# Optimization experiments

Measured on AMD Instinct MI355X. Metric: run time of the kernel, lower is better.

The kernel has to match this reference:

```python
import jax, jax.numpy as jnp
import numpy as np

N_GRAPHS = 200
NODES_PER_GRAPH = 500
N_NODES = N_GRAPHS * NODES_PER_GRAPH  # 100000
N_EDGES = 1_600_000
INPUT_DIM = 64
GCN_DIM = 128
SEQ_LEN = 20
LSTM_DIM = 128
OUTPUT_DIM = 1


def setup_inputs() -> dict:
    key = jax.random.key(0)
    ks = jax.random.split(key, 10)
    # edges constrained to stay inside each graph (block-diagonal adjacency)
    src = jax.random.randint(ks[0], (N_EDGES,), 0, N_NODES, dtype=jnp.int32)
    dst_local = jax.random.randint(ks[1], (N_EDGES,), 0, NODES_PER_GRAPH, dtype=jnp.int32)
    dst = (src // NODES_PER_GRAPH) * NODES_PER_GRAPH + dst_local
    graph_ids = jnp.arange(N_NODES, dtype=jnp.int32) // NODES_PER_GRAPH
    x = jax.random.normal(ks[2], (N_NODES, INPUT_DIM), dtype=jnp.float32)
    s = 0.05
    w_gcn = jax.random.normal(ks[3], (INPUT_DIM, GCN_DIM), dtype=jnp.float32) * s
    b_gcn = jnp.zeros((GCN_DIM,), dtype=jnp.float32)
    w_ih = jax.random.normal(ks[4], (4 * LSTM_DIM, GCN_DIM), dtype=jnp.float32) * s
    w_hh = jax.random.normal(ks[5], (4 * LSTM_DIM, LSTM_DIM), dtype=jnp.float32) * s
    b_ih = jax.random.normal(ks[6], (4 * LSTM_DIM,), dtype=jnp.float32) * s
    b_hh = jax.random.normal(ks[7], (4 * LSTM_DIM,), dtype=jnp.float32) * s
    w_fc = jax.random.normal(ks[8], (OUTPUT_DIM, LSTM_DIM), dtype=jnp.float32) * s
    b_fc = jnp.zeros((OUTPUT_DIM,), dtype=jnp.float32)
    return {"x": x, "src": src, "dst": dst, "graph_ids": graph_ids,
            "w_gcn": w_gcn, "b_gcn": b_gcn, "w_ih": w_ih, "w_hh": w_hh,
            "b_ih": b_ih, "b_hh": b_hh, "w_fc": w_fc, "b_fc": b_fc}


def reference(x, src, dst, graph_ids, w_gcn, b_gcn, w_ih, w_hh, b_ih, b_hh, w_fc, b_fc):
    ones_e = jnp.ones((src.shape[0],), dtype=x.dtype)
    # DGL GraphConv norm='both': D_out^{-1/2} on src side, D_in^{-1/2} on dst side,
    # degrees clamped to min 1 (allow_zero_in_degree=True)
    out_deg = jnp.clip(jax.ops.segment_sum(ones_e, src, num_segments=N_NODES), 1.0)
    in_deg = jnp.clip(jax.ops.segment_sum(ones_e, dst, num_segments=N_NODES), 1.0)
    h = x * (out_deg ** -0.5)[:, None]                               # [N, Din]
    agg = jax.ops.segment_sum(h[src], dst, num_segments=N_NODES)     # gather+scatter-add
    h = agg * (in_deg ** -0.5)[:, None]
    h = jnp.maximum(h @ w_gcn + b_gcn, 0.0)                           # [N, GCN_DIM], ReLU
    # dgl.mean_nodes: per-graph mean pool
    cnt = jax.ops.segment_sum(jnp.ones((N_NODES,), h.dtype), graph_ids, num_segments=N_GRAPHS)
    hg = jax.ops.segment_sum(h, graph_ids, num_segments=N_GRAPHS) / cnt[:, None]  # [T, D]
    # build_dataset: sliding windows of length SEQ_LEN over the graph time series
    B = N_GRAPHS - SEQ_LEN + 1
    idx = jnp.arange(B)[:, None] + jnp.arange(SEQ_LEN)[None, :]
    dat = hg[idx]                                                      # [B, L, D]
    # single-layer LSTM (PyTorch gate order i,f,g,o), zero initial state
    x_proj = jnp.einsum('bld,gd->blg', dat, w_ih) + b_ih               # [B, L, 4H]
    h0 = jnp.zeros((B, LSTM_DIM), dat.dtype)
    c0 = jnp.zeros((B, LSTM_DIM), dat.dtype)

    def step(carry, xt):
        hprev, cprev = carry
        gates = xt + hprev @ w_hh.T + b_hh
        i, f, g, o = jnp.split(gates, 4, axis=-1)
        c = jax.nn.sigmoid(f) * cprev + jax.nn.sigmoid(i) * jnp.tanh(g)
        hh = jax.nn.sigmoid(o) * jnp.tanh(c)
        return (hh, c), None

    (h_n, _), _ = jax.lax.scan(step, (h0, c0), jnp.swapaxes(x_proj, 0, 1))
    pred = h_n @ w_fc.T + b_fc                                         # [B, OUTPUT_DIM]
    return pred
```

## Files before the change

### kernel.cpp

```cpp
#include <hip/hip_runtime.h>
#include <hip/hip_bf16.h>

#define N_GRAPHS 200
#define NPG      500
#define NPGP     512
#define N_NODES_ 100000
#define N_EDGES_ 1600000
#define DIN      64
#define DG       128
#define SEQ      20
#define HL       128
#define G4       512
#define BWIN     (N_GRAPHS - SEQ + 1)
#define NPART    512
#define EPB      (N_EDGES_/NPART)
#define SLOTS    48
#define CAP      9216

typedef __attribute__((ext_vector_type(8))) short short8;
typedef __attribute__((ext_vector_type(4))) float float4v;
typedef __attribute__((ext_vector_type(2))) _Float16 half2v;

__device__ __forceinline__ float sigmoidf_(float v){ return 1.0f/(1.0f+expf(-v)); }

__device__ __forceinline__ unsigned short f2bf(float f) {
  unsigned int u = __float_as_uint(f);
  u += 0x7fffu + ((u >> 16) & 1u);
  return (unsigned short)(u >> 16);
}

__device__ __forceinline__ float h2dot(half2v a, half2v b, float c) {
#if __has_builtin(__builtin_amdgcn_fdot2)
  return __builtin_amdgcn_fdot2(a, b, c, false);
#else
  return c + (float)a.x*(float)b.x + (float)a.y*(float)b.y;
#endif
}

__global__ __launch_bounds__(256) void k_part(const int* __restrict__ src,
                                              const int* __restrict__ dst,
                                              const float* __restrict__ w_hh,
                                              int* __restrict__ gcount,
                                              int* __restrict__ part,
                                              int4* __restrict__ whh16) {
  __shared__ int cnt[N_GRAPHS];
  __shared__ int base[N_GRAPHS];
  __shared__ int buf[N_GRAPHS][SLOTS];
  int b = blockIdx.x, t = threadIdx.x;
  if (b < 32) {
    int i = b*256 + t;
    int k4 = i >> 9, r = i & 511;
    const float4* wp = (const float4*)(w_hh + (size_t)r*HL + k4*8);
    float4 w0 = wp[0], w1 = wp[1];
    half2v p0 = {(_Float16)w0.x, (_Float16)w0.y};
    half2v p1 = {(_Float16)w0.z, (_Float16)w0.w};
    half2v p2 = {(_Float16)w1.x, (_Float16)w1.y};
    half2v p3 = {(_Float16)w1.z, (_Float16)w1.w};
    int4 pk;
    pk.x = __builtin_bit_cast(int, p0); pk.y = __builtin_bit_cast(int, p1);
    pk.z = __builtin_bit_cast(int, p2); pk.w = __builtin_bit_cast(int, p3);
    whh16[i] = pk;
  }
  for (int g = t; g < N_GRAPHS; g += 256) cnt[g] = 0;
  __syncthreads();
  int e0 = b*EPB;
  for (int i = t; i < EPB; i += 256) {
    int s = src[e0+i], d = dst[e0+i];
    int g = s / NPG;
    int pk = ((s - g*NPG) << 9) | (d - g*NPG);
    int pos = atomicAdd(&cnt[g], 1);
    if (pos < SLOTS) buf[g][pos] = pk;
    else { int gp = atomicAdd(&gcount[g], 1); part[g*CAP + gp] = pk; }
  }
  __syncthreads();
  if (t < N_GRAPHS) base[t] = atomicAdd(&gcount[t], min(cnt[t], SLOTS));
  __syncthreads();
  int w = t >> 6, lane = t & 63;
  for (int g = w; g < N_GRAPHS; g += 4) {
    int n = min(cnt[g], SLOTS);
    if (lane < n) part[g*CAP + base[g] + lane] = buf[g][lane];
  }
}

__global__ __launch_bounds__(512) void k_sort(const int* __restrict__ gcount,
    const int* __restrict__ part,
    unsigned short* __restrict__ sorted_all,
    int* __restrict__ e_end, int* __restrict__ e_deg,
    float* __restrict__ so_g) {
  __shared__ int indeg[512], outdeg[512], off[512];
  __shared__ int wsum[8];
  __shared__ int eC[CAP];
  __shared__ unsigned short sl[CAP];
  int g = blockIdx.x, t = threadIdx.x;
  int lane = t & 63, w = t >> 6;
  indeg[t] = 0; outdeg[t] = 0;
  __syncthreads();
  int nseg = gcount[g], seg0 = g*CAP;
  for (int e = t; e < nseg; e += 512) {
    int p = part[seg0 + e];
    eC[e] = p;
    atomicAdd(&indeg[p & 511], 1);
    atomicAdd(&outdeg[p >> 9], 1);
  }
  __syncthreads();
  int v = indeg[t], sc = v;
  #pragma unroll
  for (int o = 1; o < 64; o <<= 1) { int nn = __shfl_up(sc, o); if (lane >= o) sc += nn; }
  if (lane == 63) wsum[w] = sc;
  __syncthreads();
  int woff = 0;
  #pragma unroll
  for (int i = 0; i < 8; ++i) woff += (i < w) ? wsum[i] : 0;
  off[t] = woff + sc - v;
  so_g[g*512 + t] = rsqrtf((float)max(outdeg[t], 1));
  if (t < NPG) e_deg[g*NPG + t] = v;
  __syncthreads();
  for (int e = t; e < nseg; e += 512) {
    int p = eC[e];
    int pos = atomicAdd(&off[p & 511], 1);
    sl[pos] = (unsigned short)(p >> 9);
  }
  __syncthreads();
  if (t < NPG) e_end[g*NPG + t] = seg0 + off[t];
  int n4 = nseg >> 2;
  ushort4* dv = (ushort4*)(sorted_all + seg0);
  const ushort4* sv = (const ushort4*)sl;
  for (int i = t; i < n4; i += 512) dv[i] = sv[i];
  for (int i = (n4 << 2) + t; i < nseg; i += 512) sorted_all[seg0 + i] = sl[i];
}

__global__ __launch_bounds__(512, 1) void k_aggcn(
    const float* __restrict__ x, const float* __restrict__ so_g,
    const int* __restrict__ e_end, const int* __restrict__ e_deg,
    const unsigned short* __restrict__ sorted_all,
    const float* __restrict__ w_gcn, const float* __restrict__ b_gcn,
    const float* __restrict__ w_ih, const float* __restrict__ b_ih,
    float* __restrict__ proj) {
  __shared__ __align__(16) int4 xs[4008];
  __shared__ __align__(16) int4 hpre[4096];
  __shared__ unsigned short wLds[8192];
  __shared__ float pS[1024];
  __shared__ __align__(16) float hgS[128];
  int g = blockIdx.x, t = threadIdx.x;
  int lane = t & 63, w = t >> 6;
  const float4* xg = ((const float4*)x) + (size_t)g*8000;
  const float* sog = so_g + g*512;
  ushort4* xd = (ushort4*)xs;
  for (int i = t; i < 8000; i += 512) {
    float4 vv = xg[i];
    float s2 = sog[i >> 4];
    ushort4 u;
    u.x = f2bf(vv.x*s2); u.y = f2bf(vv.y*s2); u.z = f2bf(vv.z*s2); u.w = f2bf(vv.w*s2);
    xd[i] = u;
  }
  if (t < 16) xd[8000 + t] = make_ushort4(0,0,0,0);
  for (int i = t; i < 2048; i += 512) {
    float4 w4 = ((const float4*)w_gcn)[i];
    int k = i >> 5, c4 = (i & 31) << 2;
    int h = k >> 5, j = k & 7, lhi = ((k >> 3) & 3) << 4;
    float vvv[4] = {w4.x, w4.y, w4.z, w4.w};
    #pragma unroll
    for (int u = 0; u < 4; ++u) {
      int n = c4 + u;
      int idx = ((n >> 4)*2 + h)*64 + lhi + (n & 15);
      wLds[idx*8 + j] = f2bf(vvv[u]);
    }
  }
  __syncthreads();
  int g8 = lane >> 3, fl = lane & 7;
  int G = w*8 + g8;
  for (int sI = 0; sI < 8; ++sI) {
    int nl = sI*64 + G;
    int4 outv = make_int4(0,0,0,0);
    if (nl < NPG) {
      int n = g*NPG + nl;
      int end = e_end[n], dgr = e_deg[n], st = end - dgr;
      float aHi[4] = {0.f,0.f,0.f,0.f};
      float aLo[4] = {0.f,0.f,0.f,0.f};
      int ev = (fl < dgr) ? (int)sorted_all[st + fl] : 500;
      for (int c0 = 0; c0 < dgr; c0 += 8) {
        int nc = c0 + 8;
        int evn = (nc + fl < dgr) ? (int)sorted_all[st + nc + fl] : 500;
        #pragma unroll
        for (int j = 0; j < 8; ++j) {
          int se = __shfl(ev, (g8 << 3) + j);
          int4 vv = xs[(se << 3) + fl];
          aHi[0] += __uint_as_float((unsigned)vv.x & 0xffff0000u);
          aLo[0] += __uint_as_float((unsigned)vv.x << 16);
          aHi[1] += __uint_as_float((unsigned)vv.y & 0xffff0000u);
          aLo[1] += __uint_as_float((unsigned)vv.y << 16);
          aHi[2] += __uint_as_float((unsigned)vv.z & 0xffff0000u);
          aLo[2] += __uint_as_float((unsigned)vv.z << 16);
          aHi[3] += __uint_as_float((unsigned)vv.w & 0xffff0000u);
          aLo[3] += __uint_as_float((unsigned)vv.w << 16);
        }
        ev = evn;
      }
      float sn = rsqrtf((float)max(dgr, 1));
      outv.x = (int)(((unsigned)f2bf(aLo[0]*sn)) | ((unsigned)f2bf(aHi[0]*sn) << 16));
      outv.y = (int)(((unsigned)f2bf(aLo[1]*sn)) | ((unsigned)f2bf(aHi[1]*sn) << 16));
      outv.z = (int)(((unsigned)f2bf(aLo[2]*sn)) | ((unsigned)f2bf(aHi[2]*sn) << 16));
      outv.w = (int)(((unsigned)f2bf(aLo[3]*sn)) | ((unsigned)f2bf(aHi[3]*sn) << 16));
    }
    hpre[(nl << 3) + (fl ^ (nl & 7))] = outv;
  }
  __syncthreads();
  int quad = lane >> 4, l15 = lane & 15;
  float bcol[8];
  #pragma unroll
  for (int nt = 0; nt < 8; ++nt) bcol[nt] = b_gcn[nt*16 + l15];
  float psum[8] = {0.f,0.f,0.f,0.f,0.f,0.f,0.f,0.f};
  for (int i = 0; i < 4; ++i) {
    int row0 = (w + 8*i) << 4;
    int r = row0 + l15;
    int4 a0i = hpre[(r << 3) + (quad ^ (r & 7))];
    int4 a1i = hpre[(r << 3) + ((quad + 4) ^ (r & 7))];
    short8 a0 = *(const short8*)&a0i;
    short8 a1 = *(const short8*)&a1i;
    #pragma unroll
    for (int nt = 0; nt < 8; ++nt) {
      short8 b0 = *((const short8*)&wLds[((nt*2+0)*64 + lane)*8]);
      short8 b1 = *((const short8*)&wLds[((nt*2+1)*64 + lane)*8]);
      float4v acc = {0.f, 0.f, 0.f, 0.f};
      acc = __builtin_amdgcn_mfma_f32_16x16x32_bf16(a0, b0, acc, 0, 0, 0);
      acc = __builtin_amdgcn_mfma_f32_16x16x32_bf16(a1, b1, acc, 0, 0, 0);
      #pragma unroll
      for (int r4 = 0; r4 < 4; ++r4) {
        int node = row0 + quad*4 + r4;
        float vvv = acc[r4] + bcol[nt];
        psum[nt] += (node < NPG) ? fmaxf(vvv, 0.f) : 0.f;
      }
    }
  }
  #pragma unroll
  for (int nt = 0; nt < 8; ++nt) {
    float vvv = psum[nt];
    vvv += __shfl_xor(vvv, 16);
    vvv += __shfl_xor(vvv, 32);
    if (lane < 16) pS[w*DG + nt*16 + lane] = vvv;
  }
  __syncthreads();
  if (t < DG) {
    float sum = 0.f;
    #pragma unroll
    for (int w8 = 0; w8 < 8; ++w8) sum += pS[w8*DG + t];
    hgS[t] = sum * (1.0f/NPG);
  }
  __syncthreads();
  const float4* wr = (const float4*)(w_ih + (size_t)t*HL);
  const float4* hv = (const float4*)hgS;
  float acc = b_ih[t];
  #pragma unroll
  for (int k4 = 0; k4 < 32; ++k4) {
    float4 w4 = wr[k4]; float4 h4 = hv[k4];
    acc += w4.x*h4.x + w4.y*h4.y + w4.z*h4.z + w4.w*h4.w;
  }
  proj[(size_t)g*G4 + t] = acc;
}

__global__ __launch_bounds__(512) void k_lstm(const float* __restrict__ proj,
    const int4* __restrict__ whh16, const float* __restrict__ b_hh,
    const float* __restrict__ w_fc, const float* __restrict__ b_fc,
    float* __restrict__ out) {
  __shared__ float gS[G4];
  __shared__ __align__(16) int4 hPi[16];
  int b = blockIdx.x, t = threadIdx.x;
  int4 W[16];
  #pragma unroll
  for (int k4 = 0; k4 < 16; ++k4) W[k4] = whh16[(k4 << 9) + t];
  if (t < 16) hPi[t] = make_int4(0,0,0,0);
  float bh = b_hh[t];
  float c0 = 0.f, c1 = 0.f;
  __syncthreads();
  for (int l = 0; l < SEQ; ++l) {
    float a0 = proj[(size_t)(b+l)*G4 + t] + bh;
    float a1 = 0.f, a2 = 0.f, a3 = 0.f;
    #pragma unroll
    for (int k4 = 0; k4 < 16; k4 += 4) {
      int4 hv0 = hPi[k4+0]; int4 hv1 = hPi[k4+1];
      int4 hv2 = hPi[k4+2]; int4 hv3 = hPi[k4+3];
      a0 = h2dot(__builtin_bit_cast(half2v, W[k4+0].x), __builtin_bit_cast(half2v, hv0.x), a0);
      a0 = h2dot(__builtin_bit_cast(half2v, W[k4+0].y), __builtin_bit_cast(half2v, hv0.y), a0);
      a0 = h2dot(__builtin_bit_cast(half2v, W[k4+0].z), __builtin_bit_cast(half2v, hv0.z), a0);
      a0 = h2dot(__builtin_bit_cast(half2v, W[k4+0].w), __builtin_bit_cast(half2v, hv0.w), a0);
      a1 = h2dot(__builtin_bit_cast(half2v, W[k4+1].x), __builtin_bit_cast(half2v, hv1.x), a1);
      a1 = h2dot(__builtin_bit_cast(half2v, W[k4+1].y), __builtin_bit_cast(half2v, hv1.y), a1);
      a1 = h2dot(__builtin_bit_cast(half2v, W[k4+1].z), __builtin_bit_cast(half2v, hv1.z), a1);
      a1 = h2dot(__builtin_bit_cast(half2v, W[k4+1].w), __builtin_bit_cast(half2v, hv1.w), a1);
      a2 = h2dot(__builtin_bit_cast(half2v, W[k4+2].x), __builtin_bit_cast(half2v, hv2.x), a2);
      a2 = h2dot(__builtin_bit_cast(half2v, W[k4+2].y), __builtin_bit_cast(half2v, hv2.y), a2);
      a2 = h2dot(__builtin_bit_cast(half2v, W[k4+2].z), __builtin_bit_cast(half2v, hv2.z), a2);
      a2 = h2dot(__builtin_bit_cast(half2v, W[k4+2].w), __builtin_bit_cast(half2v, hv2.w), a2);
      a3 = h2dot(__builtin_bit_cast(half2v, W[k4+3].x), __builtin_bit_cast(half2v, hv3.x), a3);
      a3 = h2dot(__builtin_bit_cast(half2v, W[k4+3].y), __builtin_bit_cast(half2v, hv3.y), a3);
      a3 = h2dot(__builtin_bit_cast(half2v, W[k4+3].z), __builtin_bit_cast(half2v, hv3.z), a3);
      a3 = h2dot(__builtin_bit_cast(half2v, W[k4+3].w), __builtin_bit_cast(half2v, hv3.w), a3);
    }
    gS[t] = (a0 + a1) + (a2 + a3);
    __syncthreads();
    if (t < 64) {
      int j0 = 2*t, j1 = 2*t + 1;
      float i0 = sigmoidf_(gS[j0]),      i1 = sigmoidf_(gS[j1]);
      float f0 = sigmoidf_(gS[HL+j0]),   f1 = sigmoidf_(gS[HL+j1]);
      float g0 = tanhf(gS[2*HL+j0]),     g1 = tanhf(gS[2*HL+j1]);
      float o0 = sigmoidf_(gS[3*HL+j0]), o1 = sigmoidf_(gS[3*HL+j1]);
      c0 = f0*c0 + i0*g0;
      c1 = f1*c1 + i1*g1;
      float h0 = o0 * tanhf(c0);
      float h1 = o1 * tanhf(c1);
      half2v hp = {(_Float16)h0, (_Float16)h1};
      ((int*)hPi)[t] = __builtin_bit_cast(int, hp);
      if (l == SEQ-1) {
        float s = h0*w_fc[j0] + h1*w_fc[j1];
        #pragma unroll
        for (int off = 32; off > 0; off >>= 1) s += __shfl_down(s, off);
        if (t == 0) out[b] = s + b_fc[0];
      }
    }
    __syncthreads();
  }
}

extern "C" void kernel_launch(void* const* d_in, const int* in_sizes, int n_in,
                              void* d_out, int out_size, void* d_ws, size_t ws_size,
                              hipStream_t stream) {
  const float* x     = (const float*)d_in[0];
  const int*   src   = (const int*)d_in[1];
  const int*   dst   = (const int*)d_in[2];
  const float* w_gcn = (const float*)d_in[4];
  const float* b_gcn = (const float*)d_in[5];
  const float* w_ih  = (const float*)d_in[6];
  const float* w_hh  = (const float*)d_in[7];
  const float* b_ih  = (const float*)d_in[8];
  const float* b_hh  = (const float*)d_in[9];
  const float* w_fc  = (const float*)d_in[10];
  const float* b_fc  = (const float*)d_in[11];
  float* out = (float*)d_out;

  char* ws = (char*)d_ws;
  size_t off = 0;
  auto alloc = [&](size_t bytes) -> void* {
    void* p = ws + off; off += (bytes + 255) & ~(size_t)255; return p;
  };
  int* gcount  = (int*)alloc((size_t)N_GRAPHS*4);
  int* part    = (int*)alloc((size_t)N_GRAPHS*CAP*4);
  unsigned short* sorted_all = (unsigned short*)alloc((size_t)N_GRAPHS*CAP*2);
  int* e_end   = (int*)alloc((size_t)N_NODES_*4);
  int* e_deg   = (int*)alloc((size_t)N_NODES_*4);
  float* so_g  = (float*)alloc((size_t)N_GRAPHS*512*4);
  int4* whh16  = (int4*)alloc((size_t)8192*16);
  float* proj  = (float*)alloc((size_t)N_GRAPHS*G4*4);
  (void)ws_size; (void)in_sizes; (void)n_in; (void)out_size;

  hipMemsetAsync(gcount, 0, (size_t)N_GRAPHS*4, stream);
  k_part<<<NPART, 256, 0, stream>>>(src, dst, w_hh, gcount, part, whh16);
  k_sort<<<N_GRAPHS, 512, 0, stream>>>(gcount, part, sorted_all, e_end, e_deg, so_g);
  k_aggcn<<<N_GRAPHS, 512, 0, stream>>>(x, so_g, e_end, e_deg, sorted_all,
                                        w_gcn, b_gcn, w_ih, b_ih, proj);
  k_lstm<<<BWIN, 512, 0, stream>>>(proj, whh16, b_hh, w_fc, b_fc, out);
}
```

Measured before the change: 188.7 us.

## Fuse per-graph edge sort into aggregation kernel and spread LSTM gates over 128 threads

Merges the per-graph counting sort and the aggregation/GCN/projection kernels into one kernel. The sorted source indices, degrees, offsets and out-degree scales now stay in shared memory instead of going through global memory, which saves one launch and a global round trip. Shared buffers are reused across phases (the weight staging goes into the sort buffer, and the partial sums go into the degree arrays). This raises LDS pressure and relies on the partial-sum buffer running past `indeg` into the adjacent `outdeg` array. The LSTM cell update now uses 128 threads, one hidden unit each, with a shuffle to pack half pairs, and adds a two-wave reduction for the final FC output.

```diff
diff --git a/kernel.cpp b/kernel.cpp
--- a/kernel.cpp
+++ b/kernel.cpp
@@ -82,23 +82,33 @@
   }
 }
 
-__global__ __launch_bounds__(512) void k_sort(const int* __restrict__ gcount,
-    const int* __restrict__ part,
-    unsigned short* __restrict__ sorted_all,
-    int* __restrict__ e_end, int* __restrict__ e_deg,
-    float* __restrict__ so_g) {
-  __shared__ int indeg[512], outdeg[512], off[512];
+__global__ __launch_bounds__(512, 1) void k_graph(
+    const int* __restrict__ gcount, const int* __restrict__ part,
+    const float* __restrict__ x,
+    const float* __restrict__ w_gcn, const float* __restrict__ b_gcn,
+    const float* __restrict__ w_ih,  const float* __restrict__ b_ih,
+    float* __restrict__ proj) {
+  __shared__ int indeg[512];
+  __shared__ int outdeg[512];
+  __shared__ int off[512];
+  __shared__ float soS[512];
   __shared__ int wsum[8];
-  __shared__ int eC[CAP];
-  __shared__ unsigned short sl[CAP];
+  __shared__ float fpS[2];
+  __shared__ unsigned short sorted[CAP];
+  __shared__ __align__(16) int4 xs[4008];
+  __shared__ __align__(16) int4 hpre[4096];
   int g = blockIdx.x, t = threadIdx.x;
   int lane = t & 63, w = t >> 6;
+
+  float4 wg[4];
+  #pragma unroll
+  for (int q = 0; q < 4; ++q) wg[q] = ((const float4*)w_gcn)[t + q*512];
+
   indeg[t] = 0; outdeg[t] = 0;
   __syncthreads();
   int nseg = gcount[g], seg0 = g*CAP;
   for (int e = t; e < nseg; e += 512) {
     int p = part[seg0 + e];
-    eC[e] = p;
     atomicAdd(&indeg[p & 511], 1);
     atomicAdd(&outdeg[p >> 9], 1);
   }
@@ -112,59 +122,22 @@
   #pragma unroll
   for (int i = 0; i < 8; ++i) woff += (i < w) ? wsum[i] : 0;
   off[t] = woff + sc - v;
-  so_g[g*512 + t] = rsqrtf((float)max(outdeg[t], 1));
-  if (t < NPG) e_deg[g*NPG + t] = v;
-  __syncthreads();
-  for (int e = t; e < nseg; e += 512) {
-    int p = eC[e];
-    int pos = atomicAdd(&off[p & 511], 1);
-    sl[pos] = (unsigned short)(p >> 9);
-  }
-  __syncthreads();
-  if (t < NPG) e_end[g*NPG + t] = seg0 + off[t];
-  int n4 = nseg >> 2;
-  ushort4* dv = (ushort4*)(sorted_all + seg0);
-  const ushort4* sv = (const ushort4*)sl;
-  for (int i = t; i < n4; i += 512) dv[i] = sv[i];
-  for (int i = (n4 << 2) + t; i < nseg; i += 512) sorted_all[seg0 + i] = sl[i];
-}
-
-__global__ __launch_bounds__(512, 1) void k_aggcn(
-    const float* __restrict__ x, const float* __restrict__ so_g,
-    const int* __restrict__ e_end, const int* __restrict__ e_deg,
-    const unsigned short* __restrict__ sorted_all,
-    const float* __restrict__ w_gcn, const float* __restrict__ b_gcn,
-    const float* __restrict__ w_ih, const float* __restrict__ b_ih,
-    float* __restrict__ proj) {
-  __shared__ __align__(16) int4 xs[4008];
-  __shared__ __align__(16) int4 hpre[4096];
-  __shared__ unsigned short wLds[8192];
-  __shared__ float pS[1024];
-  __shared__ __align__(16) float hgS[128];
-  int g = blockIdx.x, t = threadIdx.x;
-  int lane = t & 63, w = t >> 6;
+  soS[t] = rsqrtf((float)max(outdeg[t], 1));
+  __syncthreads();
   const float4* xg = ((const float4*)x) + (size_t)g*8000;
-  const float* sog = so_g + g*512;
   ushort4* xd = (ushort4*)xs;
   for (int i = t; i < 8000; i += 512) {
     float4 vv = xg[i];
-    float s2 = sog[i >> 4];
+    float s2 = soS[i >> 4];
     ushort4 u;
     u.x = f2bf(vv.x*s2); u.y = f2bf(vv.y*s2); u.z = f2bf(vv.z*s2); u.w = f2bf(vv.w*s2);
     xd[i] = u;
   }
   if (t < 16) xd[8000 + t] = make_ushort4(0,0,0,0);
-  for (int i = t; i < 2048; i += 512) {
-    float4 w4 = ((const float4*)w_gcn)[i];
-    int k = i >> 5, c4 = (i & 31) << 2;
-    int h = k >> 5, j = k & 7, lhi = ((k >> 3) & 3) << 4;
-    float vvv[4] = {w4.x, w4.y, w4.z, w4.w};
-    #pragma unroll
-    for (int u = 0; u < 4; ++u) {
-      int n = c4 + u;
-      int idx = ((n >> 4)*2 + h)*64 + lhi + (n & 15);
-      wLds[idx*8 + j] = f2bf(vvv[u]);
-    }
+  for (int e = t; e < nseg; e += 512) {
+    int p = part[seg0 + e];
+    int pos = atomicAdd(&off[p & 511], 1);
+    sorted[pos] = (unsigned short)(p >> 9);
   }
   __syncthreads();
   int g8 = lane >> 3, fl = lane & 7;
@@ -173,14 +146,13 @@
     int nl = sI*64 + G;
     int4 outv = make_int4(0,0,0,0);
     if (nl < NPG) {
-      int n = g*NPG + nl;
-      int end = e_end[n], dgr = e_deg[n], st = end - dgr;
+      int end = off[nl], dgr = indeg[nl], st = end - dgr;
       float aHi[4] = {0.f,0.f,0.f,0.f};
       float aLo[4] = {0.f,0.f,0.f,0.f};
-      int ev = (fl < dgr) ? (int)sorted_all[st + fl] : 500;
+      int ev = (fl < dgr) ? (int)sorted[st + fl] : 500;
       for (int c0 = 0; c0 < dgr; c0 += 8) {
         int nc = c0 + 8;
-        int evn = (nc + fl < dgr) ? (int)sorted_all[st + nc + fl] : 500;
+        int evn = (nc + fl < dgr) ? (int)sorted[st + nc + fl] : 500;
         #pragma unroll
         for (int j = 0; j < 8; ++j) {
           int se = __shfl(ev, (g8 << 3) + j);
@@ -205,6 +177,23 @@
     hpre[(nl << 3) + (fl ^ (nl & 7))] = outv;
   }
   __syncthreads();
+  unsigned short* wLds = (unsigned short*)sorted;
+  #pragma unroll
+  for (int q = 0; q < 4; ++q) {
+    int i = t + q*512;
+    int k = i >> 5, c4 = (i & 31) << 2;
+    int h = k >> 5, j = k & 7, lhi = ((k >> 3) & 3) << 4;
+    float vvv[4] = {wg[q].x, wg[q].y, wg[q].z, wg[q].w};
+    #pragma unroll
+    for (int u = 0; u < 4; ++u) {
+      int n = c4 + u;
+      int idx = ((n >> 4)*2 + h)*64 + lhi + (n & 15);
+      wLds[idx*8 + j] = f2bf(vvv[u]);
+    }
+  }
+  __syncthreads();
+  float* pS  = (float*)indeg;
+  float* hgS = (float*)off;
   int quad = lane >> 4, l15 = lane & 15;
   float bcol[8];
   #pragma unroll
@@ -256,6 +245,7 @@
     acc += w4.x*h4.x + w4.y*h4.y + w4.z*h4.z + w4.w*h4.w;
   }
   proj[(size_t)g*G4 + t] = acc;
+  (void)fpS;
 }
 
 __global__ __launch_bounds__(512) void k_lstm(const float* __restrict__ proj,
@@ -264,13 +254,14 @@
     float* __restrict__ out) {
   __shared__ float gS[G4];
   __shared__ __align__(16) int4 hPi[16];
+  __shared__ float fcS[2];
   int b = blockIdx.x, t = threadIdx.x;
   int4 W[16];
   #pragma unroll
   for (int k4 = 0; k4 < 16; ++k4) W[k4] = whh16[(k4 << 9) + t];
   if (t < 16) hPi[t] = make_int4(0,0,0,0);
   float bh = b_hh[t];
-  float c0 = 0.f, c1 = 0.f;
+  float c = 0.f;
   __syncthreads();
   for (int l = 0; l < SEQ; ++l) {
     float a0 = proj[(size_t)(b+l)*G4 + t] + bh;
@@ -298,27 +289,28 @@
     }
     gS[t] = (a0 + a1) + (a2 + a3);
     __syncthreads();
-    if (t < 64) {
-      int j0 = 2*t, j1 = 2*t + 1;
-      float i0 = sigmoidf_(gS[j0]),      i1 = sigmoidf_(gS[j1]);
-      float f0 = sigmoidf_(gS[HL+j0]),   f1 = sigmoidf_(gS[HL+j1]);
-      float g0 = tanhf(gS[2*HL+j0]),     g1 = tanhf(gS[2*HL+j1]);
-      float o0 = sigmoidf_(gS[3*HL+j0]), o1 = sigmoidf_(gS[3*HL+j1]);
-      c0 = f0*c0 + i0*g0;
-      c1 = f1*c1 + i1*g1;
-      float h0 = o0 * tanhf(c0);
-      float h1 = o1 * tanhf(c1);
-      half2v hp = {(_Float16)h0, (_Float16)h1};
-      ((int*)hPi)[t] = __builtin_bit_cast(int, hp);
+    if (t < 128) {
+      float iv = sigmoidf_(gS[t]);
+      float fv = sigmoidf_(gS[HL + t]);
+      float gv = tanhf(gS[2*HL + t]);
+      float ov = sigmoidf_(gS[3*HL + t]);
+      c = fv*c + iv*gv;
+      float h = ov * tanhf(c);
+      float hp2 = __shfl_xor(h, 1);
+      if (!(t & 1)) {
+        half2v hp = {(_Float16)h, (_Float16)hp2};
+        ((int*)hPi)[t >> 1] = __builtin_bit_cast(int, hp);
+      }
       if (l == SEQ-1) {
-        float s = h0*w_fc[j0] + h1*w_fc[j1];
+        float s = h * w_fc[t];
         #pragma unroll
-        for (int off = 32; off > 0; off >>= 1) s += __shfl_down(s, off);
-        if (t == 0) out[b] = s + b_fc[0];
+        for (int o = 32; o > 0; o >>= 1) s += __shfl_down(s, o);
+        if ((t & 63) == 0) fcS[t >> 6] = s;
       }
     }
     __syncthreads();
   }
+  if (t == 0) out[b] = fcS[0] + fcS[1] + b_fc[0];
 }
 
 extern "C" void kernel_launch(void* const* d_in, const int* in_sizes, int n_in,
@@ -344,18 +336,12 @@
   };
   int* gcount  = (int*)alloc((size_t)N_GRAPHS*4);
   int* part    = (int*)alloc((size_t)N_GRAPHS*CAP*4);
-  unsigned short* sorted_all = (unsigned short*)alloc((size_t)N_GRAPHS*CAP*2);
-  int* e_end   = (int*)alloc((size_t)N_NODES_*4);
-  int* e_deg   = (int*)alloc((size_t)N_NODES_*4);
-  float* so_g  = (float*)alloc((size_t)N_GRAPHS*512*4);
   int4* whh16  = (int4*)alloc((size_t)8192*16);
   float* proj  = (float*)alloc((size_t)N_GRAPHS*G4*4);
   (void)ws_size; (void)in_sizes; (void)n_in; (void)out_size;
 
   hipMemsetAsync(gcount, 0, (size_t)N_GRAPHS*4, stream);
   k_part<<<NPART, 256, 0, stream>>>(src, dst, w_hh, gcount, part, whh16);
-  k_sort<<<N_GRAPHS, 512, 0, stream>>>(gcount, part, sorted_all, e_end, e_deg, so_g);
-  k_aggcn<<<N_GRAPHS, 512, 0, stream>>>(x, so_g, e_end, e_deg, sorted_all,
-                                        w_gcn, b_gcn, w_ih, b_ih, proj);
+  k_graph<<<N_GRAPHS, 512, 0, stream>>>(gcount, part, x, w_gcn, b_gcn, w_ih, b_ih, proj);
   k_lstm<<<BWIN, 512, 0, stream>>>(proj, whh16, b_hh, w_fc, b_fc, out);
 }
```

Measured after the change: 182.6 us. -3.2%, faster.
